# Optimization experiments

Measured on AMD Instinct MI355X. Metric: run time of the kernel, lower is better.

The kernel has to match this reference:

```python
import jax, jax.numpy as jnp
import numpy as np
import math

N_NODES = 50000
N_EDGES = 640000
IN_FEATS = 128
HEADS = 8
OUT_FEATS = 16
D_FF = 4 * IN_FEATS


def setup_inputs() -> dict:
    key = jax.random.key(0)
    ks = jax.random.split(key, 10)
    s = 0.05
    return {
        "feat": jax.random.normal(ks[0], (N_NODES, IN_FEATS), jnp.float32),
        "src": jax.random.randint(ks[1], (N_EDGES,), 0, N_NODES, jnp.int32),
        "dst": jax.random.randint(ks[2], (N_EDGES,), 0, N_NODES, jnp.int32),
        "Wq": jax.random.normal(ks[3], (IN_FEATS, HEADS * OUT_FEATS), jnp.float32) * s,
        "Wk": jax.random.normal(ks[4], (IN_FEATS, HEADS * OUT_FEATS), jnp.float32) * s,
        "Wv": jax.random.normal(ks[5], (IN_FEATS, HEADS * OUT_FEATS), jnp.float32) * s,
        "ln1_g": jnp.ones((IN_FEATS,), jnp.float32),
        "ln1_b": jnp.zeros((IN_FEATS,), jnp.float32),
        "W1": jax.random.normal(ks[6], (IN_FEATS, D_FF), jnp.float32) * s,
        "b1": jnp.zeros((D_FF,), jnp.float32),
        "prelu_a": jnp.full((D_FF,), 0.25, jnp.float32),  # torch PReLU default init
        "W2": jax.random.normal(ks[7], (D_FF, IN_FEATS), jnp.float32) * s,
        "b2": jnp.zeros((IN_FEATS,), jnp.float32),
    }


def layer_norm(x, g, b, eps=1e-5):
    mu = jnp.mean(x, axis=-1, keepdims=True)
    var = jnp.mean(jnp.square(x - mu), axis=-1, keepdims=True)
    return (x - mu) * jax.lax.rsqrt(var + eps) * g + b


def reference(feat, src, dst, Wq, Wk, Wv, ln1_g, ln1_b, W1, b1, prelu_a, W2, b2):
    N = feat.shape[0]
    feat_c = jax.lax.stop_gradient(feat)  # feat.clone().detach()
    q = (feat @ Wq).reshape(N, HEADS, OUT_FEATS)
    k = (feat_c @ Wk).reshape(N, HEADS, OUT_FEATS)
    v = (feat_c @ Wv).reshape(N, HEADS, OUT_FEATS)

    # edge score: dot(k[src], q[dst]) per head -> [E, H]
    e = jnp.einsum('ehd,ehd->eh', k[src], q[dst]) / math.sqrt(OUT_FEATS * HEADS)

    # segment softmax over incoming edges of each dst node
    m = jax.ops.segment_max(e, dst, num_segments=N)          # [N, H]
    e_exp = jnp.exp(e - m[dst])                              # [E, H]
    denom = jax.ops.segment_sum(e_exp, dst, num_segments=N)  # [N, H]
    a = e_exp / denom[dst]                                   # [E, H]

    # weighted scatter-sum aggregation
    msg = v[src] * a[:, :, None]                             # [E, H, D]
    ft2 = jax.ops.segment_sum(msg, dst, num_segments=N)      # [N, H, D]

    rst = ft2.reshape(feat.shape) + feat
    # NOTE: original applies ln1 twice (ln2 is unused) -- reproduced faithfully
    rst = layer_norm(rst, ln1_g, ln1_b)
    h = rst @ W1 + b1
    h = jnp.where(h >= 0, h, prelu_a * h)                    # PReLU, per-channel
    ffn = h @ W2 + b2
    rst = layer_norm(rst + ffn, ln1_g, ln1_b)
    return rst
```

## Files before the change

### kernel.cpp

```cpp
#include <hip/hip_runtime.h>

#define N_NODES 50000
#define N_EDGES 640000
#define F 128
#define DFF 512
#define NB 196

using u32 = unsigned int;
using u16 = unsigned short;

typedef __bf16 bf16x8 __attribute__((ext_vector_type(8)));
typedef float f32x4 __attribute__((ext_vector_type(4)));
typedef float f32x2 __attribute__((ext_vector_type(2)));

__device__ __forceinline__ float bf2f(u16 u) {
    return __uint_as_float(((u32)u) << 16);
}
__device__ __forceinline__ float blo(u32 p) { return __uint_as_float(p << 16); }
__device__ __forceinline__ float bhi(u32 p) { return __uint_as_float(p & 0xffff0000u); }
__device__ __forceinline__ u16 f2bf(float f) {
    u32 u = __float_as_uint(f);
    u += 0x7fffu + ((u >> 16) & 1u);
    return (u16)(u >> 16);
}
__device__ __forceinline__ u32 pack2(float a, float b) {
    return (u32)f2bf(a) | ((u32)f2bf(b) << 16);
}

#define FEAT_UNITS (N_NODES * F / 4)
#define PH_TOTAL (FEAT_UNITS + 180224 + N_EDGES)
__global__ void k_prep(const float* __restrict__ feat, u16* __restrict__ featb,
                       const float* __restrict__ Wq, const float* __restrict__ Wk,
                       const float* __restrict__ Wv, const float* __restrict__ W1,
                       const float* __restrict__ W2, u16* __restrict__ WT,
                       const int* __restrict__ dst, int* __restrict__ cnt) {
    int idx = blockIdx.x * 256 + threadIdx.x;
    if (idx < FEAT_UNITS) {
        float4 v = reinterpret_cast<const float4*>(feat)[idx];
        uint2 p;
        p.x = pack2(v.x, v.y);
        p.y = pack2(v.z, v.w);
        reinterpret_cast<uint2*>(featb)[idx] = p;
        return;
    }
    int wi = idx - FEAT_UNITS;
    if (wi < 180224) {
        if (wi < 49152) {
            int mi = wi >> 14;
            int local = wi & 16383;
            const float* W = (mi == 0) ? Wq : ((mi == 1) ? Wk : Wv);
            int n = local >> 7, k = local & 127;
            WT[wi] = f2bf(W[(size_t)k * 128 + n]);
        } else if (wi < 114688) {
            int local = wi - 49152;
            int n = local >> 7, k = local & 127;
            WT[wi] = f2bf(W1[(size_t)k * 512 + n]);
        } else {
            int local = wi - 114688;
            int n = local >> 9, k = local & 511;
            WT[wi] = f2bf(W2[(size_t)k * 128 + n]);
        }
        return;
    }
    int e = wi - 180224;
    if (e < N_EDGES) atomicAdd(&cnt[dst[e]], 1);
}

__global__ void k_bsum(const int* __restrict__ counts, int* __restrict__ bsum) {
    int i = blockIdx.x * 256 + threadIdx.x;
    int v = (i < N_NODES) ? counts[i] : 0;
#pragma unroll
    for (int off = 32; off >= 1; off >>= 1) v += __shfl_xor(v, off, 64);
    __shared__ int ws[4];
    int lane = threadIdx.x & 63, wid = threadIdx.x >> 6;
    if (lane == 0) ws[wid] = v;
    __syncthreads();
    if (threadIdx.x == 0) bsum[blockIdx.x] = ws[0] + ws[1] + ws[2] + ws[3];
}

__global__ void k_bfill(const int* __restrict__ counts, const int* __restrict__ bsum,
                        int* __restrict__ row_ptr) {
    int b = blockIdx.x, t = threadIdx.x;
    int lane = t & 63, wid = t >> 6;
    __shared__ int ws[4];
    __shared__ int sboff[256];

    int bv = (t < NB) ? bsum[t] : 0;
    int bincl = bv;
#pragma unroll
    for (int off = 1; off < 64; off <<= 1) {
        int u = __shfl_up(bincl, off, 64);
        if (lane >= off) bincl += u;
    }
    if (lane == 63) ws[wid] = bincl;
    __syncthreads();
    int bwo = 0;
#pragma unroll
    for (int j = 0; j < 4; ++j) if (j < wid) bwo += ws[j];
    sboff[t] = bwo + bincl - bv;
    __syncthreads();
    const int boff = sboff[b];

    int i = b * 256 + t;
    int v = (i < N_NODES) ? counts[i] : 0;
    int incl = v;
#pragma unroll
    for (int off = 1; off < 64; off <<= 1) {
        int u = __shfl_up(incl, off, 64);
        if (lane >= off) incl += u;
    }
    if (lane == 63) ws[wid] = incl;
    __syncthreads();
    int wo = 0;
#pragma unroll
    for (int j = 0; j < 4; ++j) if (j < wid) wo += ws[j];
    if (i < N_NODES) row_ptr[i] = boff + wo + incl - v;
    if (i == 0) row_ptr[N_NODES] = N_EDGES;
}

__global__ void k_fill(const int* __restrict__ src, const int* __restrict__ dst,
                       const int* __restrict__ row_ptr, int* __restrict__ fill,
                       int* __restrict__ csr_src) {
    int e = blockIdx.x * 256 + threadIdx.x;
    if (e < N_EDGES) {
        int d = dst[e];
        int pos = row_ptr[d] + atomicAdd(&fill[d], 1);
        csr_src[pos] = src[e];
    }
}

template <int EPI>
__global__ __launch_bounds__(256) void k_mm(
    const u16* __restrict__ A, int lda,
    const u16* __restrict__ BT,
    void* __restrict__ Cv, int ldc,
    int K,
    const float* __restrict__ bias,
    const float* __restrict__ prelu,
    const u16* __restrict__ resid,
    const float* __restrict__ g,
    const float* __restrict__ bb)
{
    __shared__ u16 smem[17408];
    u16* sA = smem;
    u16* sB = smem + 128 * 64;
    u16* sC = smem;

    const int t = threadIdx.x;
    const int w = t >> 6;
    const int lane = t & 63;
    const int ln = lane & 15, q4 = lane >> 4;
    const int row0 = blockIdx.x * 128;
    const int cb = blockIdx.y * 128;

    if (EPI == 0 && cb != 0) {
        f32x4 acck[2][8], accv[2][8];
#pragma unroll
        for (int mt = 0; mt < 2; ++mt)
#pragma unroll
            for (int nt = 0; nt < 8; ++nt) {
                acck[mt][nt] = (f32x4){0.f, 0.f, 0.f, 0.f};
                accv[mt][nt] = (f32x4){0.f, 0.f, 0.f, 0.f};
            }
        uint4 pa[4], pb[4];
#define KV_LOAD_A(kc)                                                          \
    {                                                                          \
        _Pragma("unroll") for (int i = 0; i < 4; ++i) {                        \
            int u = i * 256 + t, r = u >> 3, k8 = (u & 7) * 8;                 \
            int row = row0 + r;                                                \
            uint4 val = make_uint4(0, 0, 0, 0);                                \
            if (row < N_NODES)                                                 \
                val = *reinterpret_cast<const uint4*>(A + (size_t)row * lda + (kc) + k8); \
            pa[i] = val;                                                       \
        }                                                                      \
    }
#define KV_LOAD_B(kc, bbase)                                                   \
    {                                                                          \
        _Pragma("unroll") for (int i = 0; i < 4; ++i) {                        \
            int u = i * 256 + t, r = u >> 3, k8 = (u & 7) * 8;                 \
            pb[i] = *reinterpret_cast<const uint4*>(BT + (size_t)((bbase) + r) * K + (kc) + k8); \
        }                                                                      \
    }
#define KV_MFMA(ACC)                                                           \
    {                                                                          \
        _Pragma("unroll") for (int ks = 0; ks < 2; ++ks) {                     \
            const int gsw = ks * 4 + q4;                                       \
            const int rA0 = w * 32 + ln;                                       \
            const int rA1 = rA0 + 16;                                          \
            bf16x8 a0 = *reinterpret_cast<const bf16x8*>(&sA[(rA0 * 8 + (gsw ^ (rA0 & 7))) * 8]); \
            bf16x8 a1 = *reinterpret_cast<const bf16x8*>(&sA[(rA1 * 8 + (gsw ^ (rA1 & 7))) * 8]); \
            _Pragma("unroll") for (int nt = 0; nt < 8; ++nt) {                 \
                const int rB = nt * 16 + ln;                                   \
                bf16x8 b = *reinterpret_cast<const bf16x8*>(&sB[(rB * 8 + (gsw ^ (rB & 7))) * 8]); \
                ACC[0][nt] = __builtin_amdgcn_mfma_f32_16x16x32_bf16(a0, b, ACC[0][nt], 0, 0, 0); \
                ACC[1][nt] = __builtin_amdgcn_mfma_f32_16x16x32_bf16(a1, b, ACC[1][nt], 0, 0, 0); \
            }                                                                  \
        }                                                                      \
    }
#pragma unroll
        for (int pass = 0; pass < 2; ++pass) {
            const int bbase = 128 + pass * 128;
            KV_LOAD_A(0);
            KV_LOAD_B(0, bbase);
            for (int kc = 0; kc < K; kc += 64) {
#pragma unroll
                for (int i = 0; i < 4; ++i) {
                    int u = i * 256 + t, r = u >> 3, gi = u & 7;
                    int off = (r * 8 + (gi ^ (r & 7))) * 8;
                    *reinterpret_cast<uint4*>(&sA[off]) = pa[i];
                    *reinterpret_cast<uint4*>(&sB[off]) = pb[i];
                }
                __syncthreads();
                if (kc + 64 < K) {
                    KV_LOAD_A(kc + 64);
                    KV_LOAD_B(kc + 64, bbase);
                }
                if (pass == 0) { KV_MFMA(acck); } else { KV_MFMA(accv); }
                __syncthreads();
            }
        }
#undef KV_LOAD_A
#undef KV_LOAD_B
#undef KV_MFMA
        u32* C32 = (u32*)Cv;
#pragma unroll
        for (int mt = 0; mt < 2; ++mt)
#pragma unroll
            for (int nt = 0; nt < 8; ++nt)
#pragma unroll
                for (int j = 0; j < 4; ++j) {
                    float kmine = bf2f(f2bf(acck[mt][nt][j]));
                    float kpair = __shfl_xor(kmine, 1, 64);
                    float vmine = bf2f(f2bf(accv[mt][nt][j]));
                    float vpair = __shfl_xor(vmine, 1, 64);
                    if ((ln & 1) == 0) {
                        int pk = __builtin_amdgcn_cvt_pk_fp8_f32(kmine, kpair, 0, false);
                        int pv = __builtin_amdgcn_cvt_pk_fp8_f32(vmine, vpair, 0, false);
                        u32 word = ((u32)pk & 0xffffu) | (((u32)pv & 0xffffu) << 16);
                        int row = row0 + w * 32 + mt * 16 + q4 * 4 + j;
                        int wd = nt * 8 + (ln >> 1);
                        if (row < N_NODES)
                            C32[(u32)row * 128u + 64u + (u32)wd] = word;
                    }
                }
        return;
    }

    f32x4 acc[2][8];
#pragma unroll
    for (int mt = 0; mt < 2; ++mt)
#pragma unroll
        for (int nt = 0; nt < 8; ++nt)
            acc[mt][nt] = (f32x4){0.f, 0.f, 0.f, 0.f};

    uint4 pa[4], pb[4];
#define LOAD_A(kc)                                                             \
    {                                                                          \
        _Pragma("unroll") for (int i = 0; i < 4; ++i) {                        \
            int u = i * 256 + t, r = u >> 3, k8 = (u & 7) * 8;                 \
            int row = row0 + r;                                                \
            uint4 val = make_uint4(0, 0, 0, 0);                                \
            if (row < N_NODES)                                                 \
                val = *reinterpret_cast<const uint4*>(A + (size_t)row * lda + (kc) + k8); \
            pa[i] = val;                                                       \
        }                                                                      \
    }
#define LOAD_B(kc)                                                             \
    {                                                                          \
        _Pragma("unroll") for (int i = 0; i < 4; ++i) {                        \
            int u = i * 256 + t, r = u >> 3, k8 = (u & 7) * 8;                 \
            pb[i] = *reinterpret_cast<const uint4*>(BT + (size_t)(cb + r) * K + (kc) + k8); \
        }                                                                      \
    }

    LOAD_A(0);
    LOAD_B(0);

    for (int kc = 0; kc < K; kc += 64) {
#pragma unroll
        for (int i = 0; i < 4; ++i) {
            int u = i * 256 + t, r = u >> 3, gi = u & 7;
            int off = (r * 8 + (gi ^ (r & 7))) * 8;
            *reinterpret_cast<uint4*>(&sA[off]) = pa[i];
            *reinterpret_cast<uint4*>(&sB[off]) = pb[i];
        }
        __syncthreads();
        if (kc + 64 < K) {
            LOAD_A(kc + 64);
            LOAD_B(kc + 64);
        }
#pragma unroll
        for (int ks = 0; ks < 2; ++ks) {
            const int gsw = ks * 4 + q4;
            const int rA0 = w * 32 + ln;
            const int rA1 = rA0 + 16;
            bf16x8 a0 = *reinterpret_cast<const bf16x8*>(&sA[(rA0 * 8 + (gsw ^ (rA0 & 7))) * 8]);
            bf16x8 a1 = *reinterpret_cast<const bf16x8*>(&sA[(rA1 * 8 + (gsw ^ (rA1 & 7))) * 8]);
#pragma unroll
            for (int nt = 0; nt < 8; ++nt) {
                const int rB = nt * 16 + ln;
                bf16x8 b = *reinterpret_cast<const bf16x8*>(&sB[(rB * 8 + (gsw ^ (rB & 7))) * 8]);
                acc[0][nt] = __builtin_amdgcn_mfma_f32_16x16x32_bf16(a0, b, acc[0][nt], 0, 0, 0);
                acc[1][nt] = __builtin_amdgcn_mfma_f32_16x16x32_bf16(a1, b, acc[1][nt], 0, 0, 0);
            }
        }
        __syncthreads();
    }
#undef LOAD_A
#undef LOAD_B

    if (EPI == 0 || EPI == 1) {
        float bs[8], pr[8];
        if (EPI == 1) {
#pragma unroll
            for (int nt = 0; nt < 8; ++nt) {
                int col = cb + nt * 16 + ln;
                bs[nt] = bias[col];
                pr[nt] = prelu[col];
            }
        }
#pragma unroll
        for (int mt = 0; mt < 2; ++mt)
#pragma unroll
            for (int nt = 0; nt < 8; ++nt)
#pragma unroll
                for (int j = 0; j < 4; ++j) {
                    float x = acc[mt][nt][j];
                    if (EPI == 1) {
                        x += bs[nt];
                        x = (x >= 0.f) ? x : pr[nt] * x;
                    }
                    sC[(w * 32 + mt * 16 + q4 * 4 + j) * 136 + nt * 16 + ln] = f2bf(x);
                }
        __syncthreads();
        u16* C = (u16*)Cv;
#pragma unroll
        for (int i = 0; i < 8; ++i) {
            int u = i * 256 + t;
            int r = u >> 4, c8 = (u & 15) * 8;
            int row = row0 + r;
            if (row < N_NODES) {
                uint4 val = *reinterpret_cast<const uint4*>(&sC[r * 136 + c8]);
                *reinterpret_cast<uint4*>(&C[(size_t)row * ldc + cb + c8]) = val;
            }
        }
    } else {
        float* C = (float*)Cv;
        float bs[8], gv[8], bv[8];
#pragma unroll
        for (int nt = 0; nt < 8; ++nt) {
            int col = nt * 16 + ln;
            bs[nt] = bias[col];
            gv[nt] = g[col];
            bv[nt] = bb[col];
        }
#pragma unroll
        for (int mt = 0; mt < 2; ++mt)
#pragma unroll
            for (int j = 0; j < 4; ++j) {
                int row = row0 + w * 32 + mt * 16 + q4 * 4 + j;
                bool ok = row < N_NODES;
                float vals[8];
                float s = 0.f, ss = 0.f;
#pragma unroll
                for (int nt = 0; nt < 8; ++nt) {
                    float x = acc[mt][nt][j] + bs[nt];
                    if (ok) x += bf2f(resid[(size_t)row * 128 + nt * 16 + ln]);
                    vals[nt] = x;
                    s += x; ss += x * x;
                }
                s += __shfl_xor(s, 8, 16); ss += __shfl_xor(ss, 8, 16);
                s += __shfl_xor(s, 4, 16); ss += __shfl_xor(ss, 4, 16);
                s += __shfl_xor(s, 2, 16); ss += __shfl_xor(ss, 2, 16);
                s += __shfl_xor(s, 1, 16); ss += __shfl_xor(ss, 1, 16);
                float mu = s * (1.f / 128.f);
                float var = ss * (1.f / 128.f) - mu * mu;
                float rs = rsqrtf(var + 1e-5f);
                if (ok) {
#pragma unroll
                    for (int nt = 0; nt < 8; ++nt)
                        C[(size_t)row * 128 + nt * 16 + ln] =
                            (vals[nt] - mu) * rs * gv[nt] + bv[nt];
                }
            }
    }
}

__global__ __launch_bounds__(256) void k_attn(
    const u32* __restrict__ Q32, const float* __restrict__ feat,
    const int* __restrict__ row_ptr, const int* __restrict__ csr_src,
    const float* __restrict__ g, const float* __restrict__ bb,
    u16* __restrict__ rstb)
{
    const int w = threadIdx.x >> 6;
    const int lane = threadIdx.x & 63;
    const int n = blockIdx.x * 4 + w;
    if (n >= N_NODES) return;
    const float scale = 0.08838834764831845f;

    const u32 qp = Q32[(u32)n * 128u + (u32)lane];
    const float q0 = blo(qp), q1 = bhi(qp);
    const int e0 = row_ptr[n], e1 = row_ptr[n + 1];
    const u32 kvlane = 64u + (u32)lane;

    float l = 0.f, a0 = 0.f, a1 = 0.f;

#define LD4(S, KV)                                                                      \
    {                                                                                   \
        KV[0] = Q32[(u32)(S).x * 128u + kvlane];                                        \
        KV[1] = Q32[(u32)(S).y * 128u + kvlane];                                        \
        KV[2] = Q32[(u32)(S).z * 128u + kvlane];                                        \
        KV[3] = Q32[(u32)(S).w * 128u + kvlane];                                        \
    }
#define CG(KV)                                                                          \
    {                                                                                   \
        f32x2 k0 = __builtin_amdgcn_cvt_pk_f32_fp8((int)KV[0], false);                  \
        f32x2 k1 = __builtin_amdgcn_cvt_pk_f32_fp8((int)KV[1], false);                  \
        f32x2 k2 = __builtin_amdgcn_cvt_pk_f32_fp8((int)KV[2], false);                  \
        f32x2 k3 = __builtin_amdgcn_cvt_pk_f32_fp8((int)KV[3], false);                  \
        float p0 = k0.x * q0 + k0.y * q1;                                               \
        float p1 = k1.x * q0 + k1.y * q1;                                               \
        float p2 = k2.x * q0 + k2.y * q1;                                               \
        float p3 = k3.x * q0 + k3.y * q1;                                               \
        p0 += __shfl_xor(p0, 4, 8); p1 += __shfl_xor(p1, 4, 8);                         \
        p2 += __shfl_xor(p2, 4, 8); p3 += __shfl_xor(p3, 4, 8);                         \
        p0 += __shfl_xor(p0, 2, 8); p1 += __shfl_xor(p1, 2, 8);                         \
        p2 += __shfl_xor(p2, 2, 8); p3 += __shfl_xor(p3, 2, 8);                         \
        p0 += __shfl_xor(p0, 1, 8); p1 += __shfl_xor(p1, 1, 8);                         \
        p2 += __shfl_xor(p2, 1, 8); p3 += __shfl_xor(p3, 1, 8);                         \
        float ea = __expf(p0 * scale), eb = __expf(p1 * scale);                         \
        float ec = __expf(p2 * scale), ed = __expf(p3 * scale);                         \
        l += (ea + eb) + (ec + ed);                                                     \
        f32x2 v0 = __builtin_amdgcn_cvt_pk_f32_fp8((int)KV[0], true);                   \
        f32x2 v1 = __builtin_amdgcn_cvt_pk_f32_fp8((int)KV[1], true);                   \
        f32x2 v2 = __builtin_amdgcn_cvt_pk_f32_fp8((int)KV[2], true);                   \
        f32x2 v3 = __builtin_amdgcn_cvt_pk_f32_fp8((int)KV[3], true);                   \
        a0 += ea * v0.x + eb * v1.x + ec * v2.x + ed * v3.x;                            \
        a1 += ea * v0.y + eb * v1.y + ec * v2.y + ed * v3.y;                            \
    }

    int e = e0;
    int rem = e1 - e0;
    {
        int4 sA, sB;
        u32 kvA[4], kvB[4];
        if (rem >= 4) {
            sA = *reinterpret_cast<const int4*>(csr_src + e);
            LD4(sA, kvA);
            if (rem >= 8) {
                sB = *reinterpret_cast<const int4*>(csr_src + e + 4);
                while (true) {
                    if (rem >= 12) sA = *reinterpret_cast<const int4*>(csr_src + e + 8);
                    LD4(sB, kvB);
                    CG(kvA);
                    e += 4; rem -= 4;
                    if (rem < 8) { CG(kvB); e += 4; rem -= 4; break; }
                    if (rem >= 12) sB = *reinterpret_cast<const int4*>(csr_src + e + 8);
                    LD4(sA, kvA);
                    CG(kvB);
                    e += 4; rem -= 4;
                    if (rem < 8) { CG(kvA); e += 4; rem -= 4; break; }
                }
            } else {
                CG(kvA);
                e += 4; rem -= 4;
            }
        }
    }
    for (; e < e1; ++e) {
        int s0 = csr_src[e];
        u32 kv = Q32[(u32)s0 * 128u + kvlane];
        f32x2 kf = __builtin_amdgcn_cvt_pk_f32_fp8((int)kv, false);
        float p0 = kf.x * q0 + kf.y * q1;
        p0 += __shfl_xor(p0, 4, 8);
        p0 += __shfl_xor(p0, 2, 8);
        p0 += __shfl_xor(p0, 1, 8);
        float ea = __expf(p0 * scale);
        f32x2 vf = __builtin_amdgcn_cvt_pk_f32_fp8((int)kv, true);
        l += ea;
        a0 += ea * vf.x;
        a1 += ea * vf.y;
    }
#undef LD4
#undef CG

    float inv = (l > 0.f) ? 1.f / l : 0.f;
    const int c2 = lane * 2;
    const float2 fr = *reinterpret_cast<const float2*>(feat + (size_t)n * 128 + c2);
    float x0 = a0 * inv + fr.x;
    float x1 = a1 * inv + fr.y;

    float sum = x0 + x1, sq = x0 * x0 + x1 * x1;
#pragma unroll
    for (int off = 32; off >= 1; off >>= 1) {
        sum += __shfl_xor(sum, off, 64);
        sq += __shfl_xor(sq, off, 64);
    }
    float mu = sum * (1.f / 128.f);
    float var = sq * (1.f / 128.f) - mu * mu;
    float rs = rsqrtf(var + 1e-5f);
    float y0 = (x0 - mu) * rs * g[c2] + bb[c2];
    float y1 = (x1 - mu) * rs * g[c2 + 1] + bb[c2 + 1];
    reinterpret_cast<u32*>(rstb)[(size_t)n * 64 + lane] = pack2(y0, y1);
}

extern "C" void kernel_launch(void* const* d_in, const int* in_sizes, int n_in,
                              void* d_out, int out_size, void* d_ws, size_t ws_size,
                              hipStream_t stream)
{
    const float* feat = (const float*)d_in[0];
    const int* src    = (const int*)d_in[1];
    const int* dst    = (const int*)d_in[2];
    const float* Wq   = (const float*)d_in[3];
    const float* Wk   = (const float*)d_in[4];
    const float* Wv   = (const float*)d_in[5];
    const float* ln_g = (const float*)d_in[6];
    const float* ln_b = (const float*)d_in[7];
    const float* W1   = (const float*)d_in[8];
    const float* b1   = (const float*)d_in[9];
    const float* pa   = (const float*)d_in[10];
    const float* W2   = (const float*)d_in[11];
    const float* b2   = (const float*)d_in[12];

    u16* qkv   = (u16*)d_ws;
    u16* h     = qkv + (size_t)N_NODES * 384;
    u16* featb = h;
    u16* rstb  = h + (size_t)N_NODES * 512;
    u16* WT    = rstb + (size_t)N_NODES * 128;
    u16* BqkvT = WT;
    u16* W1T   = WT + 49152;
    u16* W2T   = WT + 114688;
    int* counts  = (int*)(WT + 180224);
    int* fill    = counts + N_NODES;
    int* row_ptr = fill + N_NODES;
    int* csr_src = row_ptr + N_NODES + 1;
    int* bsum    = csr_src + N_EDGES;

    hipMemsetAsync(counts, 0, sizeof(int) * 2 * N_NODES, stream);
    k_prep<<<(PH_TOTAL + 255) / 256, 256, 0, stream>>>(
        feat, featb, Wq, Wk, Wv, W1, W2, WT, dst, counts);

    k_bsum<<<NB, 256, 0, stream>>>(counts, bsum);
    k_bfill<<<NB, 256, 0, stream>>>(counts, bsum, row_ptr);
    k_fill<<<(N_EDGES + 255) / 256, 256, 0, stream>>>(src, dst, row_ptr, fill, csr_src);

    const int MBK = (N_NODES + 127) / 128;

    dim3 gqkv(MBK, 2);
    k_mm<0><<<gqkv, 256, 0, stream>>>(featb, 128, BqkvT, qkv, 256, 128,
                                      nullptr, nullptr, nullptr, nullptr, nullptr);

    k_attn<<<(N_NODES + 3) / 4, 256, 0, stream>>>((const u32*)qkv, feat, row_ptr, csr_src,
                                                  ln_g, ln_b, rstb);

    dim3 gf1(MBK, 4);
    k_mm<1><<<gf1, 256, 0, stream>>>(rstb, 128, W1T, h, 512, 128,
                                     b1, pa, nullptr, nullptr, nullptr);

    dim3 gf2(MBK, 1);
    k_mm<2><<<gf2, 256, 0, stream>>>(h, 512, W2T, d_out, 128, 512,
                                     b2, nullptr, rstb, ln_g, ln_b);
}
```

Measured before the change: 305.3 us.

## Store FFN hidden activations as FP8 and expand to bf16 in second GEMM

The first FFN GEMM epilogue (bias + PReLU) now packs its output into FP8 bytes using lane shuffles and writes 4 bytes per word, instead of bf16 through shared memory. The second GEMM loads that FP8 hidden matrix, half the bytes of the earlier bf16 one, and converts it to bf16 before staging it in LDS. This cuts global traffic for the large N x 512 intermediate at the cost of conversion ALU work and reduced precision of the hidden activations.

```diff
diff --git a/kernel.cpp b/kernel.cpp
--- a/kernel.cpp
+++ b/kernel.cpp
@@ -8,6 +8,7 @@
 
 using u32 = unsigned int;
 using u16 = unsigned short;
+using u8  = unsigned char;
 
 typedef __bf16 bf16x8 __attribute__((ext_vector_type(8)));
 typedef float f32x4 __attribute__((ext_vector_type(4)));
@@ -253,7 +254,9 @@
         for (int nt = 0; nt < 8; ++nt)
             acc[mt][nt] = (f32x4){0.f, 0.f, 0.f, 0.f};
 
+    const u8* A8 = (const u8*)A;
     uint4 pa[4], pb[4];
+    uint4 pa8[2];
 #define LOAD_A(kc)                                                             \
     {                                                                          \
         _Pragma("unroll") for (int i = 0; i < 4; ++i) {                        \
@@ -265,6 +268,17 @@
             pa[i] = val;                                                       \
         }                                                                      \
     }
+#define LOAD_A8(kc)                                                            \
+    {                                                                          \
+        _Pragma("unroll") for (int i = 0; i < 2; ++i) {                        \
+            int u = i * 256 + t, r = u >> 2, g4 = u & 3;                       \
+            int row = row0 + r;                                                \
+            uint4 val = make_uint4(0, 0, 0, 0);                                \
+            if (row < N_NODES)                                                 \
+                val = *reinterpret_cast<const uint4*>(A8 + (size_t)row * 512 + (kc) + g4 * 16); \
+            pa8[i] = val;                                                      \
+        }                                                                      \
+    }
 #define LOAD_B(kc)                                                             \
     {                                                                          \
         _Pragma("unroll") for (int i = 0; i < 4; ++i) {                        \
@@ -272,21 +286,50 @@
             pb[i] = *reinterpret_cast<const uint4*>(BT + (size_t)(cb + r) * K + (kc) + k8); \
         }                                                                      \
     }
-
-    LOAD_A(0);
+#define EXPAND8(word, o0, o1)                                                  \
+    {                                                                          \
+        f32x2 lo_ = __builtin_amdgcn_cvt_pk_f32_fp8((int)(word), false);       \
+        f32x2 hi_ = __builtin_amdgcn_cvt_pk_f32_fp8((int)(word), true);        \
+        o0 = pack2(lo_.x, lo_.y);                                              \
+        o1 = pack2(hi_.x, hi_.y);                                              \
+    }
+
+    if (EPI == 2) { LOAD_A8(0); } else { LOAD_A(0); }
     LOAD_B(0);
 
     for (int kc = 0; kc < K; kc += 64) {
-#pragma unroll
-        for (int i = 0; i < 4; ++i) {
-            int u = i * 256 + t, r = u >> 3, gi = u & 7;
-            int off = (r * 8 + (gi ^ (r & 7))) * 8;
-            *reinterpret_cast<uint4*>(&sA[off]) = pa[i];
-            *reinterpret_cast<uint4*>(&sB[off]) = pb[i];
+        if (EPI == 2) {
+#pragma unroll
+            for (int i = 0; i < 2; ++i) {
+                int u = i * 256 + t, r = u >> 2, g4 = u & 3;
+                uint4 q = pa8[i];
+                u32 o0, o1, o2, o3, o4, o5, o6, o7;
+                EXPAND8(q.x, o0, o1);
+                EXPAND8(q.y, o2, o3);
+                EXPAND8(q.z, o4, o5);
+                EXPAND8(q.w, o6, o7);
+                uint4 lo = make_uint4(o0, o1, o2, o3);
+                uint4 hi = make_uint4(o4, o5, o6, o7);
+                *reinterpret_cast<uint4*>(&sA[(r * 8 + ((g4 * 2) ^ (r & 7))) * 8]) = lo;
+                *reinterpret_cast<uint4*>(&sA[(r * 8 + ((g4 * 2 + 1) ^ (r & 7))) * 8]) = hi;
+            }
+#pragma unroll
+            for (int i = 0; i < 4; ++i) {
+                int u = i * 256 + t, r = u >> 3, gi = u & 7;
+                *reinterpret_cast<uint4*>(&sB[(r * 8 + (gi ^ (r & 7))) * 8]) = pb[i];
+            }
+        } else {
+#pragma unroll
+            for (int i = 0; i < 4; ++i) {
+                int u = i * 256 + t, r = u >> 3, gi = u & 7;
+                int off = (r * 8 + (gi ^ (r & 7))) * 8;
+                *reinterpret_cast<uint4*>(&sA[off]) = pa[i];
+                *reinterpret_cast<uint4*>(&sB[off]) = pb[i];
+            }
         }
         __syncthreads();
         if (kc + 64 < K) {
-            LOAD_A(kc + 64);
+            if (EPI == 2) { LOAD_A8(kc + 64); } else { LOAD_A(kc + 64); }
             LOAD_B(kc + 64);
         }
 #pragma unroll
@@ -307,31 +350,18 @@
         __syncthreads();
     }
 #undef LOAD_A
+#undef LOAD_A8
 #undef LOAD_B
-
-    if (EPI == 0 || EPI == 1) {
-        float bs[8], pr[8];
-        if (EPI == 1) {
-#pragma unroll
-            for (int nt = 0; nt < 8; ++nt) {
-                int col = cb + nt * 16 + ln;
-                bs[nt] = bias[col];
-                pr[nt] = prelu[col];
-            }
-        }
+#undef EXPAND8
+
+    if (EPI == 0) {
 #pragma unroll
         for (int mt = 0; mt < 2; ++mt)
 #pragma unroll
             for (int nt = 0; nt < 8; ++nt)
 #pragma unroll
-                for (int j = 0; j < 4; ++j) {
-                    float x = acc[mt][nt][j];
-                    if (EPI == 1) {
-                        x += bs[nt];
-                        x = (x >= 0.f) ? x : pr[nt] * x;
-                    }
-                    sC[(w * 32 + mt * 16 + q4 * 4 + j) * 136 + nt * 16 + ln] = f2bf(x);
-                }
+                for (int j = 0; j < 4; ++j)
+                    sC[(w * 32 + mt * 16 + q4 * 4 + j) * 136 + nt * 16 + ln] = f2bf(acc[mt][nt][j]);
         __syncthreads();
         u16* C = (u16*)Cv;
 #pragma unroll
@@ -344,6 +374,35 @@
                 *reinterpret_cast<uint4*>(&C[(size_t)row * ldc + cb + c8]) = val;
             }
         }
+    } else if (EPI == 1) {
+        u32* H32 = (u32*)Cv;
+        float bs[8], pr[8];
+#pragma unroll
+        for (int nt = 0; nt < 8; ++nt) {
+            int col = cb + nt * 16 + ln;
+            bs[nt] = bias[col];
+            pr[nt] = prelu[col];
+        }
+#pragma unroll
+        for (int mt = 0; mt < 2; ++mt)
+#pragma unroll
+            for (int nt = 0; nt < 8; ++nt)
+#pragma unroll
+                for (int j = 0; j < 4; ++j) {
+                    float x = acc[mt][nt][j] + bs[nt];
+                    x = (x >= 0.f) ? x : pr[nt] * x;
+                    float xp = __shfl_xor(x, 1, 64);
+                    int p01 = __builtin_amdgcn_cvt_pk_fp8_f32(x, xp, 0, false);
+                    u32 lo16 = (u32)p01 & 0xffffu;
+                    u32 other = __shfl_xor(lo16, 2, 64);
+                    if ((ln & 3) == 0) {
+                        u32 word = lo16 | (other << 16);
+                        int row = row0 + w * 32 + mt * 16 + q4 * 4 + j;
+                        int colw = (cb + nt * 16 + ln) >> 2;
+                        if (row < N_NODES)
+                            H32[(u32)row * 128u + (u32)colw] = word;
+                    }
+                }
     } else {
         float* C = (float*)Cv;
         float bs[8], gv[8], bv[8];
```

Result: slower. 314.1 us (+2.9%).
